# Kernel tuning notes

Measured on AMD Instinct MI355X. Metric: run time of the kernel, lower is better.

The kernel has to match this reference:

```python
import jax, jax.numpy as jnp
import numpy as np

N, D = 8192, 1024
NUM_CLASSES = 128
PPC = 4  # prototypes per class
P = NUM_CLASSES * PPC
ALPHA = 1.0
EPS = 1e-9


def setup_inputs() -> dict:
    key = jax.random.key(0)
    k1, k2, k3 = jax.random.split(key, 3)
    x = jax.random.normal(k1, (N, D), dtype=jnp.float32)
    y = jax.random.randint(k2, (N,), 0, NUM_CLASSES, dtype=jnp.int64)
    prototypes = jax.random.normal(k3, (P, D), dtype=jnp.float32)
    return {"x": x, "y": y, "t_value": 1, "prototypes": prototypes}


def reference(x, y, t_value, prototypes):
    # prototype labels: i // PPC
    proto_labels = jnp.arange(P, dtype=y.dtype) // PPC  # [P]

    x_sq = jnp.sum(x * x, axis=1, keepdims=True)          # [N,1]
    p_sq = jnp.sum(prototypes * prototypes, axis=1)       # [P]
    dist = x_sq + p_sq[None, :] - 2.0 * (x @ prototypes.T)  # [N,P]

    correct_mask = proto_labels[None, :] == y[:, None]    # [N,P]
    inf = jnp.array(jnp.inf, dtype=dist.dtype)
    d1 = jnp.min(jnp.where(correct_mask, dist, inf), axis=1)   # [N]
    d2 = jnp.min(jnp.where(correct_mask, inf, dist), axis=1)   # [N]

    mu = (d1 - d2) / (d1 + d2 + EPS)
    alpha = jnp.log(1.0 + jnp.asarray(t_value, dtype=dist.dtype)) / ALPHA
    return jnp.mean(jax.nn.sigmoid(alpha * mu))
```

## Files before the change

kernel.cpp:

```cpp
#include <hip/hip_runtime.h>
#include <hip/hip_bf16.h>
#include <math.h>
#include <stdint.h>

#define NS 8192
#define DD 1024
#define NP 512
#define BK 64
#define MT 64
#define NT 128
#define NPARTS 8
#define EPSF 1e-9f
#define BIGF 3.0e38f

typedef __attribute__((ext_vector_type(8))) short bf16x8;
typedef __attribute__((ext_vector_type(4))) float f32x4;

__device__ inline unsigned short f32_to_bf16(float f) {
    uint32_t u = __builtin_bit_cast(uint32_t, f);
    uint32_t r = (u + 0x7FFFu + ((u >> 16) & 1u)) >> 16;
    return (unsigned short)r;
}

__device__ inline uint32_t cvt_pk(float lo, float hi) {
    uint32_t r;
    asm("v_cvt_pk_bf16_f32 %0, %1, %2" : "=v"(r) : "v"(lo), "v"(hi));
    return r;
}

__global__ __launch_bounds__(256) void prep_protos(
    const float* __restrict__ protos,
    unsigned short* __restrict__ pb, float* __restrict__ psq)
{
    const int row = blockIdx.x;
    const int t = threadIdx.x;
    float4 v = ((const float4*)(protos + (size_t)row * DD))[t];
    float ss = v.x * v.x + v.y * v.y + v.z * v.z + v.w * v.w;
    ushort4 o;
    o.x = f32_to_bf16(v.x); o.y = f32_to_bf16(v.y);
    o.z = f32_to_bf16(v.z); o.w = f32_to_bf16(v.w);
    ((ushort4*)(pb + (size_t)row * DD))[t] = o;
    for (int off = 32; off; off >>= 1) ss += __shfl_down(ss, off);
    __shared__ float red[4];
    if ((t & 63) == 0) red[t >> 6] = ss;
    __syncthreads();
    if (t == 0) psq[row] = red[0] + red[1] + red[2] + red[3];
}

__global__ __launch_bounds__(256, 2) void glvq_fused(
    const float* __restrict__ x, const unsigned short* __restrict__ pb,
    const float* __restrict__ psq, const int* __restrict__ y,
    float* __restrict__ d1p, float* __restrict__ d2p)
{
    __shared__ unsigned short As[2][MT * BK];
    __shared__ unsigned short Bs[2][NT * BK];
    __shared__ float xs_l[MT];

    const int tid  = threadIdx.x;
    const int lane = tid & 63;
    const int wid  = tid >> 6;
    const int wr = wid >> 1;
    const int wc = wid & 1;
    const int d    = blockIdx.x;
    const int xcd  = d & 7;
    const int slot = d >> 3;
    const int mb   = xcd * 16 + (slot & 15);
    const int nb   = slot >> 4;
    const int m0   = mb * MT;
    const int n0   = nb * NT;

    const int srow   = lane >> 3;
    const int scol16 = (lane & 7) ^ srow;
    const int sub = lane & 15, g = lane >> 4;

    const int arow = tid >> 2;
    const int acb  = (tid & 3) * 2;
    const float* xrow = x + (size_t)(m0 + arow) * DD;

    f32x4 acc[2][4] = {};
    float xss = 0.0f;
    float4 av[4];

    auto stageB = [&](int buf, int kt) {
        const int k0 = kt * BK;
#pragma unroll
        for (int j = 0; j < 4; ++j) {
            const int c = wid * 4 + j;
            const unsigned short* gb = pb + (size_t)(n0 + c * 8 + srow) * DD + k0 + scol16 * 8;
            __builtin_amdgcn_global_load_lds(
                (const __attribute__((address_space(1))) void*)gb,
                (__attribute__((address_space(3))) void*)((char*)&Bs[buf][0] + c * 1024),
                16, 0, 0);
        }
    };
    auto loadA = [&](int kt) {
#pragma unroll
        for (int j = 0; j < 2; ++j) {
            const float* p = xrow + kt * BK + (acb + j) * 8;
            av[2 * j]     = *(const float4*)(p);
            av[2 * j + 1] = *(const float4*)(p + 4);
        }
    };
    auto writeA = [&](int buf) {
#pragma unroll
        for (int j = 0; j < 2; ++j) {
            float4 u = av[2 * j], w = av[2 * j + 1];
            xss += u.x * u.x + u.y * u.y + u.z * u.z + u.w * u.w
                 + w.x * w.x + w.y * w.y + w.z * w.z + w.w * w.w;
            uint4 o;
            o.x = cvt_pk(u.x, u.y); o.y = cvt_pk(u.z, u.w);
            o.z = cvt_pk(w.x, w.y); o.w = cvt_pk(w.z, w.w);
            const int c = acb + j;
            *(uint4*)((char*)&As[buf][0] + arow * 128 + ((c ^ (arow & 7)) * 16)) = o;
        }
    };
    auto compute = [&](int buf) {
#pragma unroll
        for (int kk = 0; kk < 2; ++kk) {
            bf16x8 a[2], b[4];
#pragma unroll
            for (int m = 0; m < 2; ++m) {
                const int rowa = wr * 32 + m * 16 + sub;
                const int c16 = (kk * 4 + g) ^ (rowa & 7);
                a[m] = *(const bf16x8*)((const char*)&As[buf][0] + rowa * 128 + c16 * 16);
            }
#pragma unroll
            for (int n = 0; n < 4; ++n) {
                const int rowb = wc * 64 + n * 16 + sub;
                const int c16 = (kk * 4 + g) ^ (rowb & 7);
                b[n] = *(const bf16x8*)((const char*)&Bs[buf][0] + rowb * 128 + c16 * 16);
            }
#pragma unroll
            for (int m = 0; m < 2; ++m)
#pragma unroll
                for (int n = 0; n < 4; ++n)
                    acc[m][n] = __builtin_amdgcn_mfma_f32_16x16x32_bf16(a[m], b[n], acc[m][n], 0, 0, 0);
        }
    };

    loadA(0);
    stageB(0, 0);

    int cur = 0;
#pragma unroll 1
    for (int kt = 0; kt < DD / BK - 1; ++kt) {
        writeA(cur);
        loadA(kt + 1);
        asm volatile("s_waitcnt vmcnt(4) lgkmcnt(0)" ::: "memory");
        __builtin_amdgcn_s_barrier();
        stageB(cur ^ 1, kt + 1);
        compute(cur);
        cur ^= 1;
    }
    writeA(cur);
    asm volatile("s_waitcnt vmcnt(0) lgkmcnt(0)" ::: "memory");
    __builtin_amdgcn_s_barrier();
    compute(cur);

    xss += __shfl_xor(xss, 1);
    xss += __shfl_xor(xss, 2);
    if ((tid & 3) == 0) xs_l[arow] = xss;
    __syncthreads();

    float psqv[4];
    int   lab[4];
#pragma unroll
    for (int n = 0; n < 4; ++n) {
        const int col = n0 + wc * 64 + n * 16 + sub;
        psqv[n] = psq[col];
        lab[n]  = col >> 2;
    }
    const int part = nb * 2 + wc;
#pragma unroll
    for (int m = 0; m < 2; ++m) {
#pragma unroll
        for (int r = 0; r < 4; ++r) {
            const int rl = wr * 32 + m * 16 + g * 4 + r;
            const float xs = xs_l[rl];
            const int yy = y[m0 + rl];
            float d1 = BIGF, d2 = BIGF;
#pragma unroll
            for (int n = 0; n < 4; ++n) {
                const float dist = xs + psqv[n] - 2.0f * acc[m][n][r];
                if (lab[n] == yy) d1 = fminf(d1, dist);
                else              d2 = fminf(d2, dist);
            }
            for (int off = 8; off; off >>= 1) {
                d1 = fminf(d1, __shfl_xor(d1, off));
                d2 = fminf(d2, __shfl_xor(d2, off));
            }
            if (sub == 0) {
                d1p[part * NS + m0 + rl] = d1;
                d2p[part * NS + m0 + rl] = d2;
            }
        }
    }
}

__global__ __launch_bounds__(256) void finalize_kernel(
    const float* __restrict__ d1p, const float* __restrict__ d2p,
    const int* __restrict__ tval, float* __restrict__ bsum)
{
    const int row = blockIdx.x * 256 + threadIdx.x;
    float d1 = BIGF, d2 = BIGF;
#pragma unroll
    for (int p = 0; p < NPARTS; ++p) {
        d1 = fminf(d1, d1p[p * NS + row]);
        d2 = fminf(d2, d2p[p * NS + row]);
    }
    const float mu = (d1 - d2) / (d1 + d2 + EPSF);
    const float alpha = logf(1.0f + (float)tval[0]);
    float s = 1.0f / (1.0f + expf(-alpha * mu));
    for (int off = 32; off; off >>= 1) s += __shfl_down(s, off);
    __shared__ float red[4];
    if ((threadIdx.x & 63) == 0) red[threadIdx.x >> 6] = s;
    __syncthreads();
    if (threadIdx.x == 0) bsum[blockIdx.x] = red[0] + red[1] + red[2] + red[3];
}

__global__ void final_sum(const float* __restrict__ bsum, float* __restrict__ out) {
    float s = (threadIdx.x < NS / 256) ? bsum[threadIdx.x] : 0.0f;
    for (int off = 32; off; off >>= 1) s += __shfl_down(s, off);
    if (threadIdx.x == 0) out[0] = s * (1.0f / (float)NS);
}

extern "C" void kernel_launch(void* const* d_in, const int* in_sizes, int n_in,
                              void* d_out, int out_size, void* d_ws, size_t ws_size,
                              hipStream_t stream) {
    const float* x      = (const float*)d_in[0];
    const int*   y      = (const int*)d_in[1];
    const int*   tval   = (const int*)d_in[2];
    const float* protos = (const float*)d_in[3];
    float* out = (float*)d_out;

    char* ws = (char*)d_ws;
    unsigned short* pb = (unsigned short*)(ws);
    float* psq  = (float*)(ws + (size_t)NP * DD * 2);
    float* d1p  = psq + NP;
    float* d2p  = d1p + (size_t)NPARTS * NS;
    float* bsum = d2p + (size_t)NPARTS * NS;

    prep_protos<<<NP, 256, 0, stream>>>(protos, pb, psq);
    glvq_fused<<<(NS / MT) * (NP / NT), 256, 0, stream>>>(x, pb, psq, y, d1p, d2p);
    finalize_kernel<<<NS / 256, 256, 0, stream>>>(d1p, d2p, tval, bsum);
    final_sum<<<1, 64, 0, stream>>>(bsum, out);
}
```

Before: 34.92 us.

## Deepen GEMM pipeline to prefetch distance two with triple-buffered B tiles

Global loads of x run two k-steps ahead using two register sets. Prototype tiles go into a three-deep LDS ring via direct-to-LDS loads, and the vmcnt wait is relaxed so more memory traffic stays in flight during MFMA compute. The compute phase is also wrapped in s_setprio to favour the MFMA waves. The cost is 16KB more LDS per block, more registers for the second A staging set, and more complex prologue and epilogue handling.

Result: slower. 70.43 us (+101.7%).

```diff
diff --git a/kernel.cpp b/kernel.cpp
--- a/kernel.cpp
+++ b/kernel.cpp
@@ -9,6 +9,7 @@
 #define BK 64
 #define MT 64
 #define NT 128
+#define NSTEP (DD / BK)
 #define NPARTS 8
 #define EPSF 1e-9f
 #define BIGF 3.0e38f
@@ -53,7 +54,7 @@
     float* __restrict__ d1p, float* __restrict__ d2p)
 {
     __shared__ unsigned short As[2][MT * BK];
-    __shared__ unsigned short Bs[2][NT * BK];
+    __shared__ unsigned short Bs[3][NT * BK];
     __shared__ float xs_l[MT];
 
     const int tid  = threadIdx.x;
@@ -79,7 +80,7 @@
 
     f32x4 acc[2][4] = {};
     float xss = 0.0f;
-    float4 av[4];
+    float4 av0[4], av1[4];
 
     auto stageB = [&](int buf, int kt) {
         const int k0 = kt * BK;
@@ -93,7 +94,7 @@
                 16, 0, 0);
         }
     };
-    auto loadA = [&](int kt) {
+    auto loadA = [&](float4* av, int kt) {
 #pragma unroll
         for (int j = 0; j < 2; ++j) {
             const float* p = xrow + kt * BK + (acb + j) * 8;
@@ -101,7 +102,7 @@
             av[2 * j + 1] = *(const float4*)(p + 4);
         }
     };
-    auto writeA = [&](int buf) {
+    auto writeA = [&](int buf, const float4* av) {
 #pragma unroll
         for (int j = 0; j < 2; ++j) {
             float4 u = av[2 * j], w = av[2 * j + 1];
@@ -114,7 +115,7 @@
             *(uint4*)((char*)&As[buf][0] + arow * 128 + ((c ^ (arow & 7)) * 16)) = o;
         }
     };
-    auto compute = [&](int buf) {
+    auto compute = [&](int abuf, int bbuf) {
 #pragma unroll
         for (int kk = 0; kk < 2; ++kk) {
             bf16x8 a[2], b[4];
@@ -122,13 +123,13 @@
             for (int m = 0; m < 2; ++m) {
                 const int rowa = wr * 32 + m * 16 + sub;
                 const int c16 = (kk * 4 + g) ^ (rowa & 7);
-                a[m] = *(const bf16x8*)((const char*)&As[buf][0] + rowa * 128 + c16 * 16);
+                a[m] = *(const bf16x8*)((const char*)&As[abuf][0] + rowa * 128 + c16 * 16);
             }
 #pragma unroll
             for (int n = 0; n < 4; ++n) {
                 const int rowb = wc * 64 + n * 16 + sub;
                 const int c16 = (kk * 4 + g) ^ (rowb & 7);
-                b[n] = *(const bf16x8*)((const char*)&Bs[buf][0] + rowb * 128 + c16 * 16);
+                b[n] = *(const bf16x8*)((const char*)&Bs[bbuf][0] + rowb * 128 + c16 * 16);
             }
 #pragma unroll
             for (int m = 0; m < 2; ++m)
@@ -138,24 +139,39 @@
         }
     };
 
-    loadA(0);
-    stageB(0, 0);
-
-    int cur = 0;
+    loadA(av0, 0); stageB(0, 0);
+    loadA(av1, 1); stageB(1, 1);
+
+    int ab = 0;
+    int cb = 0;
+    int sb = 2;
 #pragma unroll 1
-    for (int kt = 0; kt < DD / BK - 1; ++kt) {
-        writeA(cur);
-        loadA(kt + 1);
-        asm volatile("s_waitcnt vmcnt(4) lgkmcnt(0)" ::: "memory");
+    for (int kt = 0; kt < NSTEP - 2; ++kt) {
+        float4* avc = (kt & 1) ? av1 : av0;
+        writeA(ab, avc);
+        loadA(avc, kt + 2);
+        asm volatile("s_waitcnt vmcnt(12) lgkmcnt(0)" ::: "memory");
         __builtin_amdgcn_s_barrier();
-        stageB(cur ^ 1, kt + 1);
-        compute(cur);
-        cur ^= 1;
-    }
-    writeA(cur);
+        stageB(sb, kt + 2);
+        __builtin_amdgcn_s_setprio(1);
+        compute(ab, cb);
+        __builtin_amdgcn_s_setprio(0);
+        ab ^= 1;
+        cb = (cb == 2) ? 0 : cb + 1;
+        sb = (sb == 2) ? 0 : sb + 1;
+    }
+    writeA(ab, (NSTEP & 1) ? av1 : av0);
+    asm volatile("s_waitcnt vmcnt(8) lgkmcnt(0)" ::: "memory");
+    __builtin_amdgcn_s_barrier();
+    __builtin_amdgcn_s_setprio(1);
+    compute(ab, cb);
+    __builtin_amdgcn_s_setprio(0);
+    ab ^= 1;
+    cb = (cb == 2) ? 0 : cb + 1;
+    writeA(ab, av1);
     asm volatile("s_waitcnt vmcnt(0) lgkmcnt(0)" ::: "memory");
     __builtin_amdgcn_s_barrier();
-    compute(cur);
+    compute(ab, cb);
 
     xss += __shfl_xor(xss, 1);
     xss += __shfl_xor(xss, 2);
```

## Load A fragments directly into registers, drop A LDS staging, double BK

Applied to the files above, without the earlier changes.

Removes the shared-memory staging of the x tile: each wave loads its fp32 A rows straight into registers in MFMA fragment layout and converts them to bf16 right before each MFMA. BK is doubled to 128 with a 16-way XOR swizzle for the B tile. The loop is hand-unrolled with two register A buffers, and s_setprio is raised around compute. This trades LDS writes and reads plus barrier work for many more VGPRs (32 float4s of A) and redundant global loads of x, since both column waves load the same rows. It also risks lower occupancy and a larger in-flight vmcnt.

Result: slower. 54.86 us (+57.1%).

```diff
diff --git a/kernel.cpp b/kernel.cpp
--- a/kernel.cpp
+++ b/kernel.cpp
@@ -6,7 +6,7 @@
 #define NS 8192
 #define DD 1024
 #define NP 512
-#define BK 64
+#define BK 128
 #define MT 64
 #define NT 128
 #define NPARTS 8
@@ -47,12 +47,39 @@
     if (t == 0) psq[row] = red[0] + red[1] + red[2] + red[3];
 }
 
+#define COMPUTE(AS, BUF)                                                         \
+    _Pragma("unroll")                                                            \
+    for (int kk = 0; kk < 4; ++kk) {                                             \
+        bf16x8 bfr[4];                                                           \
+        _Pragma("unroll")                                                        \
+        for (int n = 0; n < 4; ++n) {                                            \
+            const int rowb = wc * 64 + n * 16 + sub;                             \
+            const int c16 = (kk * 4 + g) ^ (rowb & 15);                          \
+            bfr[n] = *(const bf16x8*)((const char*)&Bs[BUF][0] + rowb * 256 + c16 * 16); \
+        }                                                                        \
+        _Pragma("unroll")                                                        \
+        for (int m = 0; m < 2; ++m) {                                            \
+            float4 u = AS[kk * 4 + m * 2], v = AS[kk * 4 + m * 2 + 1];           \
+            if (wc == 0) {                                                       \
+                float s = u.x*u.x + u.y*u.y + u.z*u.z + u.w*u.w                  \
+                        + v.x*v.x + v.y*v.y + v.z*v.z + v.w*v.w;                 \
+                if (m == 0) xss0 += s; else xss1 += s;                           \
+            }                                                                    \
+            uint4 t;                                                             \
+            t.x = cvt_pk(u.x, u.y); t.y = cvt_pk(u.z, u.w);                      \
+            t.z = cvt_pk(v.x, v.y); t.w = cvt_pk(v.z, v.w);                      \
+            bf16x8 afr = __builtin_bit_cast(bf16x8, t);                          \
+            _Pragma("unroll")                                                    \
+            for (int n = 0; n < 4; ++n)                                          \
+                acc[m][n] = __builtin_amdgcn_mfma_f32_16x16x32_bf16(afr, bfr[n], acc[m][n], 0, 0, 0); \
+        }                                                                        \
+    }
+
 __global__ __launch_bounds__(256, 2) void glvq_fused(
     const float* __restrict__ x, const unsigned short* __restrict__ pb,
     const float* __restrict__ psq, const int* __restrict__ y,
     float* __restrict__ d1p, float* __restrict__ d2p)
 {
-    __shared__ unsigned short As[2][MT * BK];
     __shared__ unsigned short Bs[2][NT * BK];
     __shared__ float xs_l[MT];
 
@@ -69,97 +96,91 @@
     const int m0   = mb * MT;
     const int n0   = nb * NT;
 
-    const int srow   = lane >> 3;
-    const int scol16 = (lane & 7) ^ srow;
     const int sub = lane & 15, g = lane >> 4;
 
-    const int arow = tid >> 2;
-    const int acb  = (tid & 3) * 2;
-    const float* xrow = x + (size_t)(m0 + arow) * DD;
-
     f32x4 acc[2][4] = {};
-    float xss = 0.0f;
-    float4 av[4];
+    float xss0 = 0.0f, xss1 = 0.0f;
+    float4 as0[16], as1[16];
+
+    const float* xr0 = x + (size_t)(m0 + wr * 32 + sub) * DD;
+    const float* xr1 = x + (size_t)(m0 + wr * 32 + 16 + sub) * DD;
 
     auto stageB = [&](int buf, int kt) {
         const int k0 = kt * BK;
 #pragma unroll
-        for (int j = 0; j < 4; ++j) {
-            const int c = wid * 4 + j;
-            const unsigned short* gb = pb + (size_t)(n0 + c * 8 + srow) * DD + k0 + scol16 * 8;
+        for (int j = 0; j < 8; ++j) {
+            const int rbase = wid * 32 + j * 4;
+            const int r = rbase + (lane >> 4);
+            const int c16 = (lane & 15) ^ (r & 15);
+            const unsigned short* gb = pb + (size_t)(n0 + r) * DD + k0 + c16 * 8;
             __builtin_amdgcn_global_load_lds(
                 (const __attribute__((address_space(1))) void*)gb,
-                (__attribute__((address_space(3))) void*)((char*)&Bs[buf][0] + c * 1024),
+                (__attribute__((address_space(3))) void*)((char*)&Bs[buf][0] + rbase * 256),
                 16, 0, 0);
         }
     };
-    auto loadA = [&](int kt) {
-#pragma unroll
-        for (int j = 0; j < 2; ++j) {
-            const float* p = xrow + kt * BK + (acb + j) * 8;
-            av[2 * j]     = *(const float4*)(p);
-            av[2 * j + 1] = *(const float4*)(p + 4);
+    auto loadA0 = [&](int kt) {
+#pragma unroll
+        for (int kk = 0; kk < 4; ++kk) {
+            const float* p0 = xr0 + kt * BK + kk * 32 + g * 8;
+            const float* p1 = xr1 + kt * BK + kk * 32 + g * 8;
+            as0[kk * 4 + 0] = *(const float4*)(p0);
+            as0[kk * 4 + 1] = *(const float4*)(p0 + 4);
+            as0[kk * 4 + 2] = *(const float4*)(p1);
+            as0[kk * 4 + 3] = *(const float4*)(p1 + 4);
         }
     };
-    auto writeA = [&](int buf) {
-#pragma unroll
-        for (int j = 0; j < 2; ++j) {
-            float4 u = av[2 * j], w = av[2 * j + 1];
-            xss += u.x * u.x + u.y * u.y + u.z * u.z + u.w * u.w
-                 + w.x * w.x + w.y * w.y + w.z * w.z + w.w * w.w;
-            uint4 o;
-            o.x = cvt_pk(u.x, u.y); o.y = cvt_pk(u.z, u.w);
-            o.z = cvt_pk(w.x, w.y); o.w = cvt_pk(w.z, w.w);
-            const int c = acb + j;
-            *(uint4*)((char*)&As[buf][0] + arow * 128 + ((c ^ (arow & 7)) * 16)) = o;
+    auto loadA1 = [&](int kt) {
+#pragma unroll
+        for (int kk = 0; kk < 4; ++kk) {
+            const float* p0 = xr0 + kt * BK + kk * 32 + g * 8;
+            const float* p1 = xr1 + kt * BK + kk * 32 + g * 8;
+            as1[kk * 4 + 0] = *(const float4*)(p0);
+            as1[kk * 4 + 1] = *(const float4*)(p0 + 4);
+            as1[kk * 4 + 2] = *(const float4*)(p1);
+            as1[kk * 4 + 3] = *(const float4*)(p1 + 4);
         }
     };
-    auto compute = [&](int buf) {
-#pragma unroll
-        for (int kk = 0; kk < 2; ++kk) {
-            bf16x8 a[2], b[4];
-#pragma unroll
-            for (int m = 0; m < 2; ++m) {
-                const int rowa = wr * 32 + m * 16 + sub;
-                const int c16 = (kk * 4 + g) ^ (rowa & 7);
-                a[m] = *(const bf16x8*)((const char*)&As[buf][0] + rowa * 128 + c16 * 16);
-            }
-#pragma unroll
-            for (int n = 0; n < 4; ++n) {
-                const int rowb = wc * 64 + n * 16 + sub;
-                const int c16 = (kk * 4 + g) ^ (rowb & 7);
-                b[n] = *(const bf16x8*)((const char*)&Bs[buf][0] + rowb * 128 + c16 * 16);
-            }
-#pragma unroll
-            for (int m = 0; m < 2; ++m)
-#pragma unroll
-                for (int n = 0; n < 4; ++n)
-                    acc[m][n] = __builtin_amdgcn_mfma_f32_16x16x32_bf16(a[m], b[n], acc[m][n], 0, 0, 0);
-        }
-    };
-
-    loadA(0);
+
+    loadA0(0);
     stageB(0, 0);
 
-    int cur = 0;
 #pragma unroll 1
-    for (int kt = 0; kt < DD / BK - 1; ++kt) {
-        writeA(cur);
-        loadA(kt + 1);
-        asm volatile("s_waitcnt vmcnt(4) lgkmcnt(0)" ::: "memory");
+    for (int kt = 0; kt < 6; kt += 2) {
+        loadA1(kt + 1);
+        asm volatile("s_waitcnt vmcnt(16)" ::: "memory");
         __builtin_amdgcn_s_barrier();
-        stageB(cur ^ 1, kt + 1);
-        compute(cur);
-        cur ^= 1;
-    }
-    writeA(cur);
-    asm volatile("s_waitcnt vmcnt(0) lgkmcnt(0)" ::: "memory");
+        stageB(1, kt + 1);
+        __builtin_amdgcn_s_setprio(1);
+        COMPUTE(as0, 0);
+        __builtin_amdgcn_s_setprio(0);
+        loadA0(kt + 2);
+        asm volatile("s_waitcnt vmcnt(16)" ::: "memory");
+        __builtin_amdgcn_s_barrier();
+        stageB(0, kt + 2);
+        __builtin_amdgcn_s_setprio(1);
+        COMPUTE(as1, 1);
+        __builtin_amdgcn_s_setprio(0);
+    }
+    loadA1(7);
+    asm volatile("s_waitcnt vmcnt(16)" ::: "memory");
     __builtin_amdgcn_s_barrier();
-    compute(cur);
-
-    xss += __shfl_xor(xss, 1);
-    xss += __shfl_xor(xss, 2);
-    if ((tid & 3) == 0) xs_l[arow] = xss;
+    stageB(1, 7);
+    __builtin_amdgcn_s_setprio(1);
+    COMPUTE(as0, 0);
+    __builtin_amdgcn_s_setprio(0);
+    asm volatile("s_waitcnt vmcnt(0)" ::: "memory");
+    __builtin_amdgcn_s_barrier();
+    __builtin_amdgcn_s_setprio(1);
+    COMPUTE(as1, 1);
+    __builtin_amdgcn_s_setprio(0);
+
+    xss0 += __shfl_xor(xss0, 16); xss0 += __shfl_xor(xss0, 32);
+    xss1 += __shfl_xor(xss1, 16); xss1 += __shfl_xor(xss1, 32);
+    if (wc == 0 && g == 0) {
+        xs_l[wr * 32 + sub]      = xss0;
+        xs_l[wr * 32 + 16 + sub] = xss1;
+    }
     __syncthreads();
 
     float psqv[4];
```
